# Optimization experiments

Measured on AMD Instinct MI355X. Metric: run time of the kernel, lower is better.

## Reference

```python
import jax, jax.numpy as jnp
import numpy as np


def setup_inputs() -> dict:
    key = jax.random.key(0)
    kq, kk, kv = jax.random.split(key, 3)
    B, S, H, HK, D = 2, 2048, 32, 8, 128
    q = jax.random.normal(kq, (B, S, H, D), dtype=jnp.float32)
    k = jax.random.normal(kk, (B, S, HK, D), dtype=jnp.float32)
    v = jax.random.normal(kv, (B, S, HK, D), dtype=jnp.float32)
    return {"q": q, "k": k, "v": v}


def reference(q, k, v):
    # Causal grouped-query attention (the math vLLM's paged attention computes
    # for a full prefill where the KV cache holds exactly this sequence).
    B, S, H, D = q.shape
    HK = k.shape[2]
    G = H // HK  # query heads per kv head
    scale = jnp.asarray(D, q.dtype) ** -0.5
    qg = q.reshape(B, S, HK, G, D)
    # scores: [B, HK, G, S(q), S(k)]
    scores = jnp.einsum("bshgd,bthd->bhgst", qg, k) * scale
    causal = jnp.tril(jnp.ones((S, S), dtype=bool))  # [Sq, Sk]
    scores = jnp.where(causal, scores, jnp.finfo(scores.dtype).min)
    probs = jax.nn.softmax(scores, axis=-1)
    out = jnp.einsum("bhgst,bthd->bshgd", probs, v)  # [B, S, HK, G, D]
    return out.reshape(B, S, H * D)
```

## Files before the change

### kernel.cpp

```cpp
#include <hip/hip_runtime.h>
#include <hip/hip_bf16.h>

typedef __attribute__((ext_vector_type(8))) short short8;
typedef __attribute__((ext_vector_type(4))) short short4v;
typedef __attribute__((ext_vector_type(4))) float f32x4;
typedef __attribute__((ext_vector_type(16))) float f32x16;

#define MFMA32(a,b,c) __builtin_amdgcn_mfma_f32_32x32x16_bf16(a,b,c,0,0,0)

static __device__ __forceinline__ short f2bf(float f){
    union{float f;unsigned u;}x; x.f=f;
    unsigned r=(x.u+0x7FFFu+((x.u>>16)&1u))>>16;
    return (short)r;
}

static __device__ __forceinline__ unsigned pkbf(float lo, float hi){
    unsigned r;
    asm("v_cvt_pk_bf16_f32 %0, %1, %2" : "=v"(r) : "v"(lo), "v"(hi));
    return r;
}

static __device__ __forceinline__ void gl_lds16(const void* g, void* l){
    __builtin_amdgcn_global_load_lds(
        (const __attribute__((address_space(1))) unsigned int*)g,
        (__attribute__((address_space(3))) unsigned int*)l, 16, 0, 0);
}

static __device__ __forceinline__ short8 pfrag(int hi,
        float e0,float e1,float e2,float e3,
        float e4,float e5,float e6,float e7){
    unsigned a01 = pkbf(e0,e1), a23 = pkbf(e2,e3);
    unsigned a45 = pkbf(e4,e5), a67 = pkbf(e6,e7);
    unsigned b01 = __shfl_xor(a01, 32);
    unsigned b23 = __shfl_xor(a23, 32);
    unsigned b45 = __shfl_xor(a45, 32);
    unsigned b67 = __shfl_xor(a67, 32);
    union{ unsigned u[4]; short8 s; } w;
    w.u[0] = hi ? b45 : a01;
    w.u[1] = hi ? b67 : a23;
    w.u[2] = hi ? a45 : b01;
    w.u[3] = hi ? a67 : b23;
    return w.s;
}

constexpr int S_=2048, H_=32, HK_=8, D_=128;
constexpr int KVBLK=64;

__global__ __launch_bounds__(256) void prep(const float* __restrict__ k, const float* __restrict__ v,
                                            short* __restrict__ kb, short* __restrict__ vt){
    __shared__ short tile[64*65];
    int bid = blockIdx.x;
    if (bid < 4096){
        int t = bid*256 + threadIdx.x;
        int e = t*4;
        int d  = e & 127;
        int hk = (e>>7) & 7;
        int s  = (e>>10) & 2047;
        int b  = e>>21;
        f32x4 x = *(const f32x4*)(k + ((size_t)((b*S_+s)*HK_+hk))*D_ + d);
        short4v o;
        o[0]=f2bf(x[0]); o[1]=f2bf(x[1]); o[2]=f2bf(x[2]); o[3]=f2bf(x[3]);
        *(short4v*)(kb + ((size_t)((b*HK_+hk)*S_+s))*D_ + d) = o;
    } else {
        bid -= 4096;
        int d0 = (bid & 1)*64;
        int s0 = ((bid>>1) & 31)*64;
        int hk = (bid>>6) & 7;
        int b  = bid>>9;
        int tid = threadIdx.x;
        #pragma unroll
        for(int i=0;i<4;i++){
            int idx = i*1024 + tid*4;
            int r = idx>>6, c = idx&63;
            f32x4 x = *(const f32x4*)(v + ((size_t)((b*S_+s0+r)*HK_+hk))*D_ + d0 + c);
            tile[(c+0)*65 + r] = f2bf(x[0]);
            tile[(c+1)*65 + r] = f2bf(x[1]);
            tile[(c+2)*65 + r] = f2bf(x[2]);
            tile[(c+3)*65 + r] = f2bf(x[3]);
        }
        __syncthreads();
        #pragma unroll
        for(int i=0;i<4;i++){
            int idx = i*1024 + tid*4;
            int dr = idx>>6, c = idx&63;
            short4v o;
            o[0]=tile[dr*65+c]; o[1]=tile[dr*65+c+1]; o[2]=tile[dr*65+c+2]; o[3]=tile[dr*65+c+3];
            *(short4v*)(vt + ((size_t)((b*HK_+hk)*D_ + d0+dr))*S_ + s0 + c) = o;
        }
    }
}

__global__ __launch_bounds__(256,2) void attn_fwd(
    const float* __restrict__ q, const short* __restrict__ kb,
    const short* __restrict__ vtb, float* __restrict__ out)
{
    __shared__ __align__(16) unsigned char kls[2][KVBLK*D_*2];
    __shared__ __align__(16) unsigned char vls[2][D_*KVBLK*2];

    const int bid  = blockIdx.x;
    const int wg   = (bid & 7)*64 + (bid >> 3);
    const int kvg  = wg >> 5;
    const int b    = kvg >> 3;
    const int hk   = kvg & 7;
    const int rr_  = wg & 31;
    const int h    = hk*4 + (rr_ >> 3);
    const int pair = rr_ & 7;

    const int tid  = threadIdx.x;
    const int wave = tid >> 6;
    const int ln   = tid & 31;
    const int hi   = (tid >> 5) & 1;

    const float qscale = 0.08838834764831845f * 1.4426950408889634f;

    const short* kt_base = kb  + (size_t)(b*HK_+hk)*S_*D_;
    const short* vt_base = vtb + (size_t)(b*HK_+hk)*D_*S_;

    auto STAGE = [&](int bufi, int kvt){
        const char* kg = (const char*)(kt_base + (size_t)kvt*KVBLK*D_);
        #pragma unroll
        for(int i=0;i<4;i++){
            int p = (i*256 + tid)*16;
            int src = p ^ (((p>>8)&7)<<4);
            gl_lds16(kg + src, &kls[bufi][p]);
        }
        const char* vg = (const char*)vt_base + (size_t)kvt*KVBLK*2;
        #pragma unroll
        for(int i=0;i<4;i++){
            int p = (i*256 + tid)*16;
            int d = p>>7;
            int src = (p&127) ^ ((d&7)<<4);
            gl_lds16(vg + (size_t)d*(S_*2) + src, &vls[bufi][p]);
        }
    };

    int cur = 0;
    STAGE(0, 0);
    __syncthreads();

    for(int phase=0; phase<2; ++phase){
        const int c      = phase ? pair : 15-pair;
        const int nkv    = 2*c + 2;
        const int kvmaxw = 2*c + (wave >> 1);
        const int qg     = c*128 + wave*32 + ln;

        short8 qf[8];
        {
            const float* qp = q + ((size_t)(b*S_ + qg)*H_ + h)*D_;
            #pragma unroll
            for(int kk=0;kk<8;kk++){
                int d0 = kk*16 + hi*8;
                f32x4 a = *(const f32x4*)(qp + d0);
                f32x4 cc= *(const f32x4*)(qp + d0 + 4);
                union{ unsigned u[4]; short8 s; } w;
                w.u[0]=pkbf(a[0]*qscale, a[1]*qscale);
                w.u[1]=pkbf(a[2]*qscale, a[3]*qscale);
                w.u[2]=pkbf(cc[0]*qscale, cc[1]*qscale);
                w.u[3]=pkbf(cc[2]*qscale, cc[3]*qscale);
                qf[kk]=w.s;
            }
        }

        f32x16 oac[4];
        #pragma unroll
        for(int dt=0;dt<4;dt++) oac[dt] = (f32x16)0.f;
        float l = 0.f;

        for(int kvt=0; kvt<nkv; ++kvt){
            int nxt = (kvt+1 < nkv) ? (kvt+1) : (phase==0 ? 0 : -1);
            if (nxt >= 0) STAGE(cur^1, nxt);

            if (kvt <= kvmaxw){
                const int kv0 = kvt*64;
                f32x16 sa0=(f32x16)0.f, sa1=(f32x16)0.f;
                const int sz = (ln&7)<<4;
                #pragma unroll
                for(int kk=0;kk<8;kk++){
                    int cb = kk*32 + hi*16;
                    short8 k0 = *(const short8*)&kls[cur][(ln*256 + cb) ^ sz];
                    short8 k1 = *(const short8*)&kls[cur][((ln+32)*256 + cb) ^ sz];
                    sa0 = MFMA32(k0, qf[kk], sa0);
                    sa1 = MFMA32(k1, qf[kk], sa1);
                }
                if (kv0 + 63 > c*128 + wave*32){
                    #pragma unroll
                    for(int r=0;r<16;r++){
                        int kvl = (r&3) + 8*(r>>2) + 4*hi;
                        if (kv0 + kvl      > qg) sa0[r] = -1e30f;
                        if (kv0 + 32 + kvl > qg) sa1[r] = -1e30f;
                    }
                }
                float ps0=0.f, ps1=0.f, ps2=0.f, ps3=0.f;
                #pragma unroll
                for(int r=0;r<16;r+=4){
                    sa0[r+0]=__builtin_amdgcn_exp2f(sa0[r+0]); ps0+=sa0[r+0];
                    sa0[r+1]=__builtin_amdgcn_exp2f(sa0[r+1]); ps1+=sa0[r+1];
                    sa0[r+2]=__builtin_amdgcn_exp2f(sa0[r+2]); ps2+=sa0[r+2];
                    sa0[r+3]=__builtin_amdgcn_exp2f(sa0[r+3]); ps3+=sa0[r+3];
                }
                #pragma unroll
                for(int r=0;r<16;r+=4){
                    sa1[r+0]=__builtin_amdgcn_exp2f(sa1[r+0]); ps0+=sa1[r+0];
                    sa1[r+1]=__builtin_amdgcn_exp2f(sa1[r+1]); ps1+=sa1[r+1];
                    sa1[r+2]=__builtin_amdgcn_exp2f(sa1[r+2]); ps2+=sa1[r+2];
                    sa1[r+3]=__builtin_amdgcn_exp2f(sa1[r+3]); ps3+=sa1[r+3];
                }
                float ps = (ps0+ps1)+(ps2+ps3);
                l += ps + __shfl_xor(ps, 32);
                short8 pa0 = pfrag(hi, sa0[0],sa0[1],sa0[2], sa0[3], sa0[4], sa0[5], sa0[6], sa0[7]);
                short8 pa1 = pfrag(hi, sa0[8],sa0[9],sa0[10],sa0[11],sa0[12],sa0[13],sa0[14],sa0[15]);
                short8 pa2 = pfrag(hi, sa1[0],sa1[1],sa1[2], sa1[3], sa1[4], sa1[5], sa1[6], sa1[7]);
                short8 pa3 = pfrag(hi, sa1[8],sa1[9],sa1[10],sa1[11],sa1[12],sa1[13],sa1[14],sa1[15]);
                #pragma unroll
                for(int dt=0;dt<4;dt++){
                    int rb = (dt*32 + ln)*128;
                    short8 v0 = *(const short8*)&vls[cur][(rb +   0 + hi*16) ^ sz];
                    oac[dt] = MFMA32(v0, pa0, oac[dt]);
                    short8 v1 = *(const short8*)&vls[cur][(rb +  32 + hi*16) ^ sz];
                    oac[dt] = MFMA32(v1, pa1, oac[dt]);
                    short8 v2 = *(const short8*)&vls[cur][(rb +  64 + hi*16) ^ sz];
                    oac[dt] = MFMA32(v2, pa2, oac[dt]);
                    short8 v3 = *(const short8*)&vls[cur][(rb +  96 + hi*16) ^ sz];
                    oac[dt] = MFMA32(v3, pa3, oac[dt]);
                }
            }
            __syncthreads();
            cur ^= 1;
        }

        float rinv = 1.0f / l;
        float* op = out + ((size_t)(b*S_ + qg)*H_ + h)*D_;
        #pragma unroll
        for(int dt=0;dt<4;dt++){
            #pragma unroll
            for(int rr=0;rr<4;rr++){
                f32x4 o4;
                o4[0]=oac[dt][rr*4+0]*rinv;
                o4[1]=oac[dt][rr*4+1]*rinv;
                o4[2]=oac[dt][rr*4+2]*rinv;
                o4[3]=oac[dt][rr*4+3]*rinv;
                *(f32x4*)(op + dt*32 + rr*8 + hi*4) = o4;
            }
        }
    }
}

extern "C" void kernel_launch(void* const* d_in, const int* in_sizes, int n_in,
                              void* d_out, int out_size, void* d_ws, size_t ws_size,
                              hipStream_t stream) {
    const float* q = (const float*)d_in[0];
    const float* k = (const float*)d_in[1];
    const float* v = (const float*)d_in[2];
    float* out = (float*)d_out;

    short* kb = (short*)d_ws;
    short* vt = (short*)((char*)d_ws + (size_t)2*HK_*S_*D_*2);

    prep<<<dim3(4096+1024), dim3(256), 0, stream>>>(k, v, kb, vt);
    attn_fwd<<<dim3(512), dim3(256), 0, stream>>>(q, kb, vt, out);
}
```

Before: 112.0 us.

## Permute V-transpose layout so P fragments pack without cross-lane shuffles

The prep kernel now writes the transposed V with a permuted column order within each 16-element group, swapping the middle 4-element chunks. Because V's key order now matches the register order of the score accumulators, the P operand can be packed directly from each lane's own values. This removes the per-iteration __shfl_xor exchanges and selects from the softmax-to-PV path. The row-sum reduction across half-waves is deferred to a single shuffle at the end. The cost is coupling the V layout to the MFMA register mapping.

Measured after the change: 103.8 us (median of 2 runs). 1.08x faster.

```diff
diff --git a/kernel.cpp b/kernel.cpp
--- a/kernel.cpp
+++ b/kernel.cpp
@@ -26,22 +26,10 @@
         (__attribute__((address_space(3))) unsigned int*)l, 16, 0, 0);
 }
 
-static __device__ __forceinline__ short8 pfrag(int hi,
-        float e0,float e1,float e2,float e3,
-        float e4,float e5,float e6,float e7){
-    unsigned a01 = pkbf(e0,e1), a23 = pkbf(e2,e3);
-    unsigned a45 = pkbf(e4,e5), a67 = pkbf(e6,e7);
-    unsigned b01 = __shfl_xor(a01, 32);
-    unsigned b23 = __shfl_xor(a23, 32);
-    unsigned b45 = __shfl_xor(a45, 32);
-    unsigned b67 = __shfl_xor(a67, 32);
-    union{ unsigned u[4]; short8 s; } w;
-    w.u[0] = hi ? b45 : a01;
-    w.u[1] = hi ? b67 : a23;
-    w.u[2] = hi ? a45 : b01;
-    w.u[3] = hi ? a67 : b23;
-    return w.s;
-}
+#define PACK8(s, b) ({ union{unsigned u[4]; short8 v;} w_;           \
+    w_.u[0]=pkbf((s)[(b)+0],(s)[(b)+1]); w_.u[1]=pkbf((s)[(b)+2],(s)[(b)+3]); \
+    w_.u[2]=pkbf((s)[(b)+4],(s)[(b)+5]); w_.u[3]=pkbf((s)[(b)+6],(s)[(b)+7]); \
+    w_.v; })
 
 constexpr int S_=2048, H_=32, HK_=8, D_=128;
 constexpr int KVBLK=64;
@@ -85,7 +73,9 @@
             int dr = idx>>6, c = idx&63;
             short4v o;
             o[0]=tile[dr*65+c]; o[1]=tile[dr*65+c+1]; o[2]=tile[dr*65+c+2]; o[3]=tile[dr*65+c+3];
-            *(short4v*)(vt + ((size_t)((b*HK_+hk)*D_ + d0+dr))*S_ + s0 + c) = o;
+            int m  = c & 12;
+            int cp = (m==4 || m==8) ? (c ^ 12) : c;
+            *(short4v*)(vt + ((size_t)((b*HK_+hk)*D_ + d0+dr))*S_ + s0 + cp) = o;
         }
     }
 }
@@ -205,12 +195,11 @@
                     sa1[r+2]=__builtin_amdgcn_exp2f(sa1[r+2]); ps2+=sa1[r+2];
                     sa1[r+3]=__builtin_amdgcn_exp2f(sa1[r+3]); ps3+=sa1[r+3];
                 }
-                float ps = (ps0+ps1)+(ps2+ps3);
-                l += ps + __shfl_xor(ps, 32);
-                short8 pa0 = pfrag(hi, sa0[0],sa0[1],sa0[2], sa0[3], sa0[4], sa0[5], sa0[6], sa0[7]);
-                short8 pa1 = pfrag(hi, sa0[8],sa0[9],sa0[10],sa0[11],sa0[12],sa0[13],sa0[14],sa0[15]);
-                short8 pa2 = pfrag(hi, sa1[0],sa1[1],sa1[2], sa1[3], sa1[4], sa1[5], sa1[6], sa1[7]);
-                short8 pa3 = pfrag(hi, sa1[8],sa1[9],sa1[10],sa1[11],sa1[12],sa1[13],sa1[14],sa1[15]);
+                l += (ps0+ps1)+(ps2+ps3);
+                short8 pa0 = PACK8(sa0, 0);
+                short8 pa1 = PACK8(sa0, 8);
+                short8 pa2 = PACK8(sa1, 0);
+                short8 pa3 = PACK8(sa1, 8);
                 #pragma unroll
                 for(int dt=0;dt<4;dt++){
                     int rb = (dt*32 + ln)*128;
@@ -228,7 +217,8 @@
             cur ^= 1;
         }
 
-        float rinv = 1.0f / l;
+        float lt = l + __shfl_xor(l, 32);
+        float rinv = 1.0f / lt;
         float* op = out + ((size_t)(b*S_ + qg)*H_ + h)*D_;
         #pragma unroll
         for(int dt=0;dt<4;dt++){
```
